# Kernel optimization log

Measured on AMD Instinct MI355X. Metric: run time of the kernel, lower is better.

## Reference

```python
import jax, jax.numpy as jnp
import numpy as np

WS, SHIFT, NH = 7, 3, 12

def _rel_pos_index(ws):
    coords = np.stack(np.meshgrid(np.arange(ws), np.arange(ws), indexing='ij'))  # [2,ws,ws]
    coords = coords.reshape(2, -1)
    rel = (coords[:, :, None] - coords[:, None, :]).transpose(1, 2, 0)  # [N,N,2]
    rel[:, :, 0] += ws - 1
    rel[:, :, 1] += ws - 1
    rel[:, :, 0] *= 2 * ws - 1
    return rel.sum(-1)  # [N,N] ints in [0,(2ws-1)^2)

def _attn_mask(H, W, ws, shift):
    img = np.zeros((H, W))
    cnt = 0
    for h in (slice(0, -ws), slice(-ws, -shift), slice(-shift, None)):
        for w in (slice(0, -ws), slice(-ws, -shift), slice(-shift, None)):
            img[h, w] = cnt
            cnt += 1
    mw = img.reshape(H // ws, ws, W // ws, ws).transpose(0, 2, 1, 3).reshape(-1, ws * ws)
    diff = mw[:, None, :] - mw[:, :, None]  # unsqueeze(1)-unsqueeze(2)
    return np.where(diff != 0, -100.0, 0.0).astype(np.float32)  # [nW,N,N]

def setup_inputs() -> dict:
    key = jax.random.key(0)
    ks = jax.random.split(key, 16)
    B, C, H, W = 16, 384, 56, 56
    hid = 4 * C
    s = 0.02
    return {
        'x': jax.random.normal(ks[0], (B, C, H, W), jnp.float32),
        'qkv_w': jax.random.normal(ks[1], (3 * C, C), jnp.float32) * s,
        'qkv_b': jnp.zeros((3 * C,), jnp.float32),
        'proj_w': jax.random.normal(ks[2], (C, C), jnp.float32) * s,
        'proj_b': jnp.zeros((C,), jnp.float32),
        'rpb': jax.random.normal(ks[3], ((2 * WS - 1) ** 2, NH), jnp.float32) * s,
        'norm1_w': jnp.ones((C,), jnp.float32),
        'norm1_b': jnp.zeros((C,), jnp.float32),
        'norm2_w': jnp.ones((C,), jnp.float32),
        'norm2_b': jnp.zeros((C,), jnp.float32),
        'fc1_w': jax.random.normal(ks[4], (hid, C), jnp.float32) * s,
        'fc1_b': jnp.zeros((hid,), jnp.float32),
        'fc2_w': jax.random.normal(ks[5], (C, hid), jnp.float32) * s,
        'fc2_b': jnp.zeros((C,), jnp.float32),
    }

def _ln(v, w, b):
    m = v.mean(-1, keepdims=True)
    var = ((v - m) ** 2).mean(-1, keepdims=True)
    return (v - m) / jnp.sqrt(var + 1e-5) * w + b

def reference(x, qkv_w, qkv_b, proj_w, proj_b, rpb, norm1_w, norm1_b, norm2_w, norm2_b, fc1_w, fc1_b, fc2_w, fc2_b):
    B, C, H, W = x.shape
    ws, shift, nh = WS, SHIFT, NH
    hd = C // nh
    scale = hd ** -0.5
    N = ws * ws
    nwh, nww = H // ws, W // ws
    xt = x.reshape(B, C, H * W).transpose(0, 2, 1)  # [B,L,C]
    shortcut = xt
    xn = _ln(xt, norm1_w, norm1_b).reshape(B, H, W, C)
    xs = jnp.roll(xn, (-shift, -shift), axis=(1, 2))
    win = xs.reshape(B, nwh, ws, nww, ws, C).transpose(0, 1, 3, 2, 4, 5).reshape(-1, N, C)
    qkv = (win @ qkv_w.T + qkv_b).reshape(-1, N, 3, nh, hd).transpose(2, 0, 3, 1, 4)
    q, k, v = qkv[0] * scale, qkv[1], qkv[2]  # [nWtot,nh,N,hd]
    attn = jnp.einsum('whnd,whmd->whnm', q, k)
    rpi = jnp.asarray(_rel_pos_index(ws))
    bias = rpb[rpi.reshape(-1)].reshape(N, N, nh).transpose(2, 0, 1)
    attn = attn + bias[None]
    mask = jnp.asarray(_attn_mask(H, W, ws, shift))  # [nW,N,N]
    nW = mask.shape[0]
    attn = attn.reshape(B, nW, nh, N, N) + mask[None, :, None]
    attn = jax.nn.softmax(attn.reshape(-1, nh, N, N), axis=-1)
    out = jnp.einsum('whnm,whmd->whnd', attn, v).transpose(0, 2, 1, 3).reshape(-1, N, C)
    out = out @ proj_w.T + proj_b
    out = out.reshape(B, nwh, nww, ws, ws, C).transpose(0, 1, 3, 2, 4, 5).reshape(B, H, W, C)
    out = jnp.roll(out, (shift, shift), axis=(1, 2)).reshape(B, H * W, C)
    xres = shortcut + out
    h = _ln(xres, norm2_w, norm2_b)
    h = jax.nn.gelu(h @ fc1_w.T + fc1_b, approximate=False)
    h = h @ fc2_w.T + fc2_b
    xout = xres + h
    return xout.transpose(0, 2, 1).reshape(B, C, H, W)
```

## Files before the change

### kernel.cpp

```cpp
#include <hip/hip_runtime.h>


using US   = unsigned short;
using bf8  = __attribute__((ext_vector_type(8))) short;
using f4   = __attribute__((ext_vector_type(4))) float;
using u4   = __attribute__((ext_vector_type(4))) unsigned int;
using u2   = __attribute__((ext_vector_type(2))) unsigned int;

__device__ __forceinline__ float b2f(US h){
  union { unsigned u; float f; } v; v.u = ((unsigned)h) << 16; return v.f;
}
__device__ __forceinline__ US f2b(float f){
  union { float f; unsigned u; } v; v.f = f;
  unsigned r = (v.u + 0x7FFFu + ((v.u >> 16) & 1u)) >> 16;
  return (US)r;
}
__device__ __forceinline__ unsigned cvt_pk_bf16(float lo, float hi){
  unsigned r;
  asm("v_cvt_pk_bf16_f32 %0, %1, %2" : "=v"(r) : "v"(lo), "v"(hi));
  return r;
}
__device__ __forceinline__ float rcp_f(float x){
  float r; asm("v_rcp_f32 %0, %1" : "=v"(r) : "v"(x)); return r;
}
__device__ __forceinline__ float exp2_f(float x){
  float r; asm("v_exp_f32 %0, %1" : "=v"(r) : "v"(x)); return r;
}
__device__ __forceinline__ float gelu_f(float x){
  float t = x*x;
  float m = x * (-2.3022082f - 0.1029434f*t);
  float e = exp2_f(m);
  return x * rcp_f(1.f + e);
}
__device__ __forceinline__ int xcd_seq(int n, int nwg){
  int q = nwg >> 3, r = nwg & 7;
  int xcd = n & 7, idx = n >> 3;
  int base = (xcd < r) ? xcd*(q+1) : (r + xcd*q);
  return base + idx;
}

__global__ void k_detect(const unsigned* __restrict__ n1w, int* __restrict__ flag){
  *flag = (n1w[0] == 0x3F803F80u) ? 1 : 0;
}

struct Ptrs { const void* p[13]; };
__constant__ const int g_cnt[13] = {442368,1152,147456,384,2028,384,384,384,384,589824,1536,589824,384};
__constant__ const int g_off[13] = {0,442368,443520,590976,591360,593408,593792,594176,594560,
                                    594944,1184768,1186304,1776128};

__global__ __launch_bounds__(256) void k_convert_all(Ptrs ptrs, US* __restrict__ dst,
                                                     const int* __restrict__ flag, int totpair){
  const int f = *flag;
  int g = blockIdx.x*256 + threadIdx.x;
  const int stride = gridDim.x*256;
  for (; g < totpair; g += stride){
    int i = 0, base = 0, off = 0;
    #pragma unroll
    for (int t = 0; t < 13; t++){
      int np = g_cnt[t] >> 1;
      if (g >= base && g < base + np){ i = t; off = base; }
      base += np;
    }
    int li = g - off;
    unsigned* d = (unsigned*)dst + (g_off[i] >> 1);
    if (f){
      d[li] = ((const unsigned*)ptrs.p[i])[li];
    } else {
      const float* s = (const float*)ptrs.p[i];
      unsigned lo = f2b(s[2*li]), hi = f2b(s[2*li+1]);
      d[li] = lo | (hi << 16);
    }
  }
}

__global__ __launch_bounds__(256) void k_transpose(const void* __restrict__ x, size_t xoff,
                                                   US* __restrict__ xt, const int* __restrict__ flag){
  __shared__ float tile[32][33];
  const int f = *flag;
  const int b = blockIdx.z;
  const int l0 = blockIdx.x * 32, c0 = blockIdx.y * 32;
  const int tx = threadIdx.x, ty = threadIdx.y;
  #pragma unroll
  for (int i = 0; i < 4; i++){
    int c = c0 + ty + i*8;
    size_t idx = xoff + ((size_t)b*384 + c)*3136 + l0 + tx;
    tile[ty + i*8][tx] = f ? b2f(((const US*)x)[idx]) : ((const float*)x)[idx];
  }
  __syncthreads();
  #pragma unroll
  for (int i = 0; i < 4; i++){
    int l = l0 + ty + i*8;
    xt[((size_t)b*3136 + l)*384 + c0 + tx] = f2b(tile[tx][ty + i*8]);
  }
}

__device__ __forceinline__ int win_row(int row){
  int b = row / 3136, l = row - b*3136;
  int ho = l / 56, wo = l - ho*56;
  int hs = ho - 3; if (hs < 0) hs += 56;
  int wsc = wo - 3; if (wsc < 0) wsc += 56;
  return ((b*8 + hs/7)*8 + wsc/7)*49 + (hs%7)*7 + (wsc%7);
}

__global__ __launch_bounds__(256) void k_ln1(const US* __restrict__ xt, const US* __restrict__ g,
                                             const US* __restrict__ bb, US* __restrict__ Xw){
  const int wv = threadIdx.x >> 6, lane = threadIdx.x & 63;
  const int row = blockIdx.x*4 + wv;
  const unsigned* src = (const unsigned*)(xt + (size_t)row*384);
  float v[6]; float s1 = 0.f, s2 = 0.f;
  #pragma unroll
  for (int k = 0; k < 3; k++){
    unsigned u = src[lane + 64*k];
    float lo = b2f((US)(u & 0xffff)), hi = b2f((US)(u >> 16));
    v[2*k] = lo; v[2*k+1] = hi;
    s1 += lo + hi; s2 += lo*lo + hi*hi;
  }
  #pragma unroll
  for (int off = 1; off < 64; off <<= 1){ s1 += __shfl_xor(s1, off); s2 += __shfl_xor(s2, off); }
  float mean = s1 * (1.f/384.f);
  float var  = s2 * (1.f/384.f) - mean*mean;
  float rstd = rsqrtf(var + 1e-5f);
  int r = win_row(row);
  unsigned* dst = (unsigned*)(Xw + (size_t)r*384);
  const unsigned* gw = (const unsigned*)g;
  const unsigned* gb = (const unsigned*)bb;
  #pragma unroll
  for (int k = 0; k < 3; k++){
    unsigned wg = gw[lane + 64*k], wb = gb[lane + 64*k];
    float o0 = (v[2*k]   - mean)*rstd*b2f((US)(wg & 0xffff)) + b2f((US)(wb & 0xffff));
    float o1 = (v[2*k+1] - mean)*rstd*b2f((US)(wg >> 16))    + b2f((US)(wb >> 16));
    dst[lane + 64*k] = cvt_pk_bf16(o0, o1);
  }
}

template<int EPI, int KT, int LDA>
__global__ __launch_bounds__(256) void k_gemm(const US* __restrict__ A, const US* __restrict__ Bw,
                                              const US* __restrict__ bias, US* __restrict__ C,
                                              int N){
  __shared__ __align__(16) US sh[128*128];
  US* Asl = sh;
  US* Bsl = sh + 8192;
  const int tid = threadIdx.x, wv = tid >> 6, lane = tid & 63;
  const int l16 = lane & 15, lq = lane >> 4;
  const int GX = gridDim.x, GY = gridDim.y;
  const int s  = xcd_seq(blockIdx.x + GX*blockIdx.y, GX*GY);
  const int bx = s / GY, by = s - bx*GY;
  const int row0 = bx * 128, col0 = by * 128;
  const int wr = (wv >> 1) * 64, wc = (wv & 1) * 64;
  f4 acc[4][4] = {};
  const int r8 = lane >> 3;
  const int c8 = lane & 7;
  const int csrc = c8 ^ r8;
  const US* ga = A  + (size_t)(row0 + wv*32 + r8)*LDA + csrc*8;
  const US* gb = Bw + (size_t)(col0 + wv*32 + r8)*KT  + csrc*8;
  US* lA = Asl + wv*2048;
  US* lB = Bsl + wv*2048;
  const int x7   = l16 & 7;
  #pragma unroll
  for (int k0 = 0; k0 < KT; k0 += 64){
    #pragma unroll
    for (int i = 0; i < 4; i++){
      __builtin_amdgcn_global_load_lds((__attribute__((address_space(1))) void*)(ga + k0 + (size_t)i*8*LDA),
                                       (__attribute__((address_space(3))) void*)(lA + i*512), 16, 0, 0);
      __builtin_amdgcn_global_load_lds((__attribute__((address_space(1))) void*)(gb + k0 + (size_t)i*8*KT),
                                       (__attribute__((address_space(3))) void*)(lB + i*512), 16, 0, 0);
    }
    __syncthreads();
    #pragma unroll
    for (int kk = 0; kk < 2; kk++){
      const int coff = (((kk << 2) | lq) ^ x7) * 8;
      bf8 af[4], bfr[4];
      #pragma unroll
      for (int m = 0; m < 4; m++) af[m]  = *(const bf8*)(Asl + (wr + m*16 + l16)*64 + coff);
      #pragma unroll
      for (int n = 0; n < 4; n++) bfr[n] = *(const bf8*)(Bsl + (wc + n*16 + l16)*64 + coff);
      #pragma unroll
      for (int n = 0; n < 4; n++)
        #pragma unroll
        for (int m = 0; m < 4; m++)
          acc[n][m] = __builtin_amdgcn_mfma_f32_16x16x32_bf16(bfr[n], af[m], acc[n][m], 0, 0, 0);
    }
    __syncthreads();
  }
  #pragma unroll
  for (int n = 0; n < 4; n++){
    const int colt = wc + n*16 + lq*4;
    const int colb = col0 + colt;
    u2 bw = *(const u2*)(bias + colb);
    float bv[4] = { b2f((US)(bw[0] & 0xffff)), b2f((US)(bw[0] >> 16)),
                    b2f((US)(bw[1] & 0xffff)), b2f((US)(bw[1] >> 16)) };
    #pragma unroll
    for (int m = 0; m < 4; m++){
      const int rowt = wr + m*16 + l16;
      float v[4];
      #pragma unroll
      for (int j = 0; j < 4; j++){
        float val = acc[n][m][j] + bv[j];
        if (EPI == 1){ if (colb < 384) val *= 0.17677669529663687f; }
        if (EPI == 2){ val = gelu_f(val); }
        v[j] = val;
      }
      u2 w;
      w[0] = cvt_pk_bf16(v[0], v[1]);
      w[1] = cvt_pk_bf16(v[2], v[3]);
      *(u2*)(sh + rowt*128 + (((colt >> 3) ^ (rowt & 15)) << 3) + (colt & 7)) = w;
    }
  }
  __syncthreads();
  const int cr = tid & 15, rb = tid >> 4;
  #pragma unroll
  for (int it = 0; it < 8; it++){
    const int r = rb + it*16;
    u4 v = *(const u4*)(sh + r*128 + ((cr ^ (r & 15)) << 3));
    *(u4*)(C + (size_t)(row0 + r)*N + col0 + cr*8) = v;
  }
}

__global__ __launch_bounds__(64) void k_attn(US* QKV, const US* __restrict__ rpb){
  const int s = xcd_seq(blockIdx.x + 12*blockIdx.y, 12*gridDim.y);
  const int win = s / 12, head = s - win*12;
  const int lane = threadIdx.x;
  const int l16 = lane & 15, lq = lane >> 4;
  __shared__ __align__(16) US ps[64*72];
  __shared__ float biasl[169];

  for (int i = lane; i < 169; i += 64) biasl[i] = b2f(rpb[i*12 + head]);
  __syncthreads();

  const size_t rowbase = (size_t)win * 49;
  const US* Qb = QKV + rowbase*1152 + head*32;

  bf8 qf[4], kf[4];
  #pragma unroll
  for (int m = 0; m < 4; m++){
    int row = m*16 + l16; if (row > 48) row = 48;
    const US* p = Qb + (size_t)row*1152 + lq*8;
    qf[m] = *(const bf8*)p;
    kf[m] = *(const bf8*)(p + 384);
  }

  const f4 zacc = {0.f, 0.f, 0.f, 0.f};
  f4 s4[4][4];
  #pragma unroll
  for (int m = 0; m < 4; m++)
    #pragma unroll
    for (int n = 0; n < 4; n++)
      s4[m][n] = __builtin_amdgcn_mfma_f32_16x16x32_bf16(qf[m], kf[n], zacc, 0, 0, 0);

  bf8 vf[2][2];
  #pragma unroll
  for (int kk = 0; kk < 2; kk++)
    #pragma unroll
    for (int i = 0; i < 8; i++){
      int key = kk*32 + lq*8 + i; if (key > 48) key = 48;
      const US* vp = Qb + (size_t)key*1152 + 768;
      vf[0][kk][i] = (short)vp[l16];
      vf[1][kk][i] = (short)vp[16 + l16];
    }

  const int wh = (win >> 3) & 7, ww = win & 7;
  int i2a[4], j2a[4], lblm[4]; bool vm[4];
  #pragma unroll
  for (int n = 0; n < 4; n++){
    int mk = n*16 + l16;
    vm[n] = (mk < 49);
    int mkc = vm[n] ? mk : 48;
    int i2 = mkc / 7, j2 = mkc - 7*i2;
    i2a[n] = i2; j2a[n] = j2;
    lblm[n] = ((wh == 7) ? (i2 < 4 ? 3 : 6) : 0) + ((ww == 7) ? (j2 < 4 ? 1 : 2) : 0);
  }

  float rinv[4][4];
  #pragma unroll
  for (int m = 0; m < 4; m++){
    #pragma unroll
    for (int j = 0; j < 4; j++){
      int nq = m*16 + lq*4 + j;
      int nqc = nq < 49 ? nq : 48;
      int i1 = nqc / 7, j1 = nqc - 7*i1;
      int lblq = ((wh == 7) ? (i1 < 4 ? 3 : 6) : 0) + ((ww == 7) ? (j1 < 4 ? 1 : 2) : 0);
      float vals[4];
      #pragma unroll
      for (int n = 0; n < 4; n++){
        int relidx = (i1 - i2a[n] + 6)*13 + (j1 - j2a[n] + 6);
        float t = s4[m][n][j] + biasl[relidx];
        if (lblq != lblm[n]) t -= 100.f;
        if (!vm[n]) t = -1e30f;
        vals[n] = t;
      }
      float mv = fmaxf(fmaxf(vals[0], vals[1]), fmaxf(vals[2], vals[3]));
      #pragma unroll
      for (int off = 1; off < 16; off <<= 1) mv = fmaxf(mv, __shfl_xor(mv, off));
      float sum = 0.f;
      #pragma unroll
      for (int n = 0; n < 4; n++){
        float p = vm[n] ? __expf(vals[n] - mv) : 0.f;
        sum += p;
        ps[(size_t)(m*16 + lq*4 + j)*72 + n*16 + l16] = f2b(p);
      }
      #pragma unroll
      for (int off = 1; off < 16; off <<= 1) sum += __shfl_xor(sum, off);
      rinv[m][j] = rcp_f(sum);
    }
  }
  __syncthreads();

  f4 o[4][2] = {};
  #pragma unroll
  for (int m = 0; m < 4; m++){
    #pragma unroll
    for (int kk = 0; kk < 2; kk++){
      bf8 pf = *(const bf8*)(ps + (size_t)(m*16 + l16)*72 + kk*32 + lq*8);
      #pragma unroll
      for (int nb = 0; nb < 2; nb++)
        o[m][nb] = __builtin_amdgcn_mfma_f32_16x16x32_bf16(pf, vf[nb][kk], o[m][nb], 0, 0, 0);
    }
  }
  #pragma unroll
  for (int m = 0; m < 4; m++)
    #pragma unroll
    for (int nb = 0; nb < 2; nb++)
      #pragma unroll
      for (int j = 0; j < 4; j++){
        int nq = m*16 + lq*4 + j;
        if (nq < 49){
          int d = nb*16 + l16;
          QKV[(rowbase + nq)*1152 + head*32 + d] = f2b(o[m][nb][j] * rinv[m][j]);
        }
      }
}

__global__ __launch_bounds__(256) void k_res_ln2(US* xt, const US* __restrict__ Y,
                                                 const US* __restrict__ g, const US* __restrict__ bb,
                                                 US* __restrict__ Xm){
  const int wv = threadIdx.x >> 6, lane = threadIdx.x & 63;
  const int row = blockIdx.x*4 + wv;
  int r = win_row(row);
  unsigned* sa = (unsigned*)(xt + (size_t)row*384);
  const unsigned* sy = (const unsigned*)(Y  + (size_t)r*384);
  unsigned* dm = (unsigned*)(Xm   + (size_t)row*384);
  float v[6]; float s1 = 0.f, s2 = 0.f;
  #pragma unroll
  for (int k = 0; k < 3; k++){
    unsigned ua = sa[lane + 64*k], uy = sy[lane + 64*k];
    float lo = b2f((US)(ua & 0xffff)) + b2f((US)(uy & 0xffff));
    float hi = b2f((US)(ua >> 16))    + b2f((US)(uy >> 16));
    v[2*k] = lo; v[2*k+1] = hi;
    s1 += lo + hi; s2 += lo*lo + hi*hi;
    sa[lane + 64*k] = cvt_pk_bf16(lo, hi);
  }
  #pragma unroll
  for (int off = 1; off < 64; off <<= 1){ s1 += __shfl_xor(s1, off); s2 += __shfl_xor(s2, off); }
  float mean = s1 * (1.f/384.f);
  float var  = s2 * (1.f/384.f) - mean*mean;
  float rstd = rsqrtf(var + 1e-5f);
  const unsigned* gw = (const unsigned*)g;
  const unsigned* gb = (const unsigned*)bb;
  #pragma unroll
  for (int k = 0; k < 3; k++){
    unsigned wg = gw[lane + 64*k], wb = gb[lane + 64*k];
    float o0 = (v[2*k]   - mean)*rstd*b2f((US)(wg & 0xffff)) + b2f((US)(wb & 0xffff));
    float o1 = (v[2*k+1] - mean)*rstd*b2f((US)(wg >> 16))    + b2f((US)(wb >> 16));
    dm[lane + 64*k] = cvt_pk_bf16(o0, o1);
  }
}

__global__ __launch_bounds__(256) void k_final(const US* __restrict__ xres, const US* __restrict__ Z,
                                               void* __restrict__ out, size_t ooff,
                                               const int* __restrict__ flag){
  __shared__ float tile[32][33];
  const int f = *flag;
  const int b = blockIdx.z;
  const int l0 = blockIdx.x * 32, c0 = blockIdx.y * 32;
  const int tx = threadIdx.x, ty = threadIdx.y;
  #pragma unroll
  for (int i = 0; i < 4; i++){
    int l = l0 + ty + i*8;
    size_t idx = ((size_t)b*3136 + l)*384 + c0 + tx;
    tile[ty + i*8][tx] = b2f(xres[idx]) + b2f(Z[idx]);
  }
  __syncthreads();
  #pragma unroll
  for (int i = 0; i < 4; i++){
    int c = c0 + ty + i*8;
    size_t idx = ooff + ((size_t)b*384 + c)*3136 + l0 + tx;
    float v = tile[tx][ty + i*8];
    if (f) ((US*)out)[idx] = f2b(v);
    else   ((float*)out)[idx] = v;
  }
}

extern "C" void kernel_launch(void* const* d_in, const int* in_sizes, int n_in,
                              void* d_out, int out_size, void* d_ws, size_t ws_size,
                              hipStream_t stream){
  char* w = (char*)d_ws;
  int* flag = (int*)w;
  US*  Wb   = (US*)(w + 256);

  const size_t O_QKVW=0, O_QKVB=442368, O_PROJW=443520, O_PROJB=590976, O_RPB=591360,
               O_N1W=593408, O_N1B=593792, O_N2W=594176, O_N2B=594560,
               O_FC1W=594944, O_FC1B=1184768, O_FC2W=1186304, O_FC2B=1776128;

  k_detect<<<1, 1, 0, stream>>>((const unsigned*)d_in[6], flag);
  {
    Ptrs ptrs;
    for (int i = 0; i < 13; i++) ptrs.p[i] = d_in[i+1];
    int totpair = (442368+1152+147456+384+2028+384*4+589824+1536+589824+384)/2;
    int grid = (totpair + 255)/256;
    k_convert_all<<<grid, 256, 0, stream>>>(ptrs, Wb, flag, totpair);
  }

  const size_t WOFF = 4ull<<20;
  const size_t U1 = 2408448ull;
  int NBC = 16;
  while (NBC > 4 && WOFF + 6ull*U1*(size_t)NBC > ws_size) NBC >>= 1;
  const size_t U  = U1 * (size_t)NBC;
  const int rows  = NBC * 3136;
  const int nchunks = 16 / NBC;

  char* cw = w + WOFF;
  US* xt  = (US*)(cw);
  US* Xw  = (US*)(cw + U);
  US* Xm  = Xw;
  US* QKV = (US*)(cw + 2*U);
  US* Hb  = (US*)(cw + 2*U);
  US* Zc  = (US*)(cw + 4*U);
  US* Y   = (US*)(cw + 5*U);

  dim3 bt(32, 8);
  for (int ch = 0; ch < nchunks; ch++){
    size_t eoff = (size_t)ch * NBC * 384 * 3136;
    k_transpose<<<dim3(98, 12, NBC), bt, 0, stream>>>(d_in[0], eoff, xt, flag);
    k_ln1<<<rows/4, 256, 0, stream>>>(xt, Wb+O_N1W, Wb+O_N1B, Xw);
    k_gemm<1,384,384><<<dim3(rows/128, 9), 256, 0, stream>>>(Xw, Wb+O_QKVW, Wb+O_QKVB, QKV, 1152);
    k_attn<<<dim3(12, NBC*64), 64, 0, stream>>>(QKV, Wb+O_RPB);
    k_gemm<0,384,1152><<<dim3(rows/128, 3), 256, 0, stream>>>(QKV, Wb+O_PROJW, Wb+O_PROJB, Y, 384);
    k_res_ln2<<<rows/4, 256, 0, stream>>>(xt, Y, Wb+O_N2W, Wb+O_N2B, Xm);
    const int Mh = rows / 2;
    for (int h = 0; h < 2; h++){
      k_gemm<2,384,384><<<dim3(Mh/128, 12), 256, 0, stream>>>(Xm + (size_t)h*Mh*384, Wb+O_FC1W, Wb+O_FC1B, Hb, 1536);
      k_gemm<0,1536,1536><<<dim3(Mh/128, 3), 256, 0, stream>>>(Hb, Wb+O_FC2W, Wb+O_FC2B, Zc + (size_t)h*Mh*384, 384);
    }
    k_final<<<dim3(98, 12, NBC), bt, 0, stream>>>(xt, Zc, d_out, eoff, flag);
  }
}
```

Measured before the change: 416.6 us.

## Fuse transpose with LN1, fold residual into proj epilogue, prescale Q weights

```diff
diff --git a/kernel.cpp b/kernel.cpp
--- a/kernel.cpp
+++ b/kernel.cpp
@@ -62,80 +62,83 @@
       base += np;
     }
     int li = g - off;
+    const bool qs = (i == 0 && li < 73728) || (i == 1 && li < 192);
+    const float sc = qs ? 0.17677669529663687f : 1.0f;
     unsigned* d = (unsigned*)dst + (g_off[i] >> 1);
     if (f){
-      d[li] = ((const unsigned*)ptrs.p[i])[li];
+      unsigned u = ((const unsigned*)ptrs.p[i])[li];
+      if (qs){
+        float lo = b2f((US)(u & 0xffff)) * sc, hi = b2f((US)(u >> 16)) * sc;
+        u = (unsigned)f2b(lo) | ((unsigned)f2b(hi) << 16);
+      }
+      d[li] = u;
     } else {
       const float* s = (const float*)ptrs.p[i];
-      unsigned lo = f2b(s[2*li]), hi = f2b(s[2*li+1]);
+      unsigned lo = f2b(s[2*li] * sc), hi = f2b(s[2*li+1] * sc);
       d[li] = lo | (hi << 16);
     }
   }
 }
 
-__global__ __launch_bounds__(256) void k_transpose(const void* __restrict__ x, size_t xoff,
-                                                   US* __restrict__ xt, const int* __restrict__ flag){
-  __shared__ float tile[32][33];
+__global__ __launch_bounds__(256) void k_pre(const void* __restrict__ x, size_t xoff,
+                                             US* __restrict__ xt, US* __restrict__ Xw,
+                                             const US* __restrict__ g, const US* __restrict__ bb,
+                                             const int* __restrict__ flag){
+  __shared__ float T[32][385];
   const int f = *flag;
-  const int b = blockIdx.z;
-  const int l0 = blockIdx.x * 32, c0 = blockIdx.y * 32;
+  const int b = blockIdx.y;
+  const int l0 = blockIdx.x * 32;
   const int tx = threadIdx.x, ty = threadIdx.y;
   #pragma unroll
-  for (int i = 0; i < 4; i++){
-    int c = c0 + ty + i*8;
-    size_t idx = xoff + ((size_t)b*384 + c)*3136 + l0 + tx;
-    tile[ty + i*8][tx] = f ? b2f(((const US*)x)[idx]) : ((const float*)x)[idx];
+  for (int cy = 0; cy < 12; cy++){
+    #pragma unroll
+    for (int i = 0; i < 4; i++){
+      int c = cy*32 + ty + i*8;
+      size_t idx = xoff + ((size_t)b*384 + c)*3136 + l0 + tx;
+      T[tx][c] = f ? b2f(((const US*)x)[idx]) : ((const float*)x)[idx];
+    }
   }
   __syncthreads();
-  #pragma unroll
-  for (int i = 0; i < 4; i++){
-    int l = l0 + ty + i*8;
-    xt[((size_t)b*3136 + l)*384 + c0 + tx] = f2b(tile[tx][ty + i*8]);
-  }
-}
-
-__device__ __forceinline__ int win_row(int row){
-  int b = row / 3136, l = row - b*3136;
-  int ho = l / 56, wo = l - ho*56;
-  int hs = ho - 3; if (hs < 0) hs += 56;
-  int wsc = wo - 3; if (wsc < 0) wsc += 56;
-  return ((b*8 + hs/7)*8 + wsc/7)*49 + (hs%7)*7 + (wsc%7);
-}
-
-__global__ __launch_bounds__(256) void k_ln1(const US* __restrict__ xt, const US* __restrict__ g,
-                                             const US* __restrict__ bb, US* __restrict__ Xw){
-  const int wv = threadIdx.x >> 6, lane = threadIdx.x & 63;
-  const int row = blockIdx.x*4 + wv;
-  const unsigned* src = (const unsigned*)(xt + (size_t)row*384);
-  float v[6]; float s1 = 0.f, s2 = 0.f;
-  #pragma unroll
-  for (int k = 0; k < 3; k++){
-    unsigned u = src[lane + 64*k];
-    float lo = b2f((US)(u & 0xffff)), hi = b2f((US)(u >> 16));
-    v[2*k] = lo; v[2*k+1] = hi;
-    s1 += lo + hi; s2 += lo*lo + hi*hi;
-  }
-  #pragma unroll
-  for (int off = 1; off < 64; off <<= 1){ s1 += __shfl_xor(s1, off); s2 += __shfl_xor(s2, off); }
-  float mean = s1 * (1.f/384.f);
-  float var  = s2 * (1.f/384.f) - mean*mean;
-  float rstd = rsqrtf(var + 1e-5f);
-  int r = win_row(row);
-  unsigned* dst = (unsigned*)(Xw + (size_t)r*384);
+  const int tid = ty*32 + tx;
+  const int wv = tid >> 6, lane = tid & 63;
   const unsigned* gw = (const unsigned*)g;
   const unsigned* gb = (const unsigned*)bb;
-  #pragma unroll
-  for (int k = 0; k < 3; k++){
-    unsigned wg = gw[lane + 64*k], wb = gb[lane + 64*k];
-    float o0 = (v[2*k]   - mean)*rstd*b2f((US)(wg & 0xffff)) + b2f((US)(wb & 0xffff));
-    float o1 = (v[2*k+1] - mean)*rstd*b2f((US)(wg >> 16))    + b2f((US)(wb >> 16));
-    dst[lane + 64*k] = cvt_pk_bf16(o0, o1);
+  for (int rr = 0; rr < 8; rr++){
+    const int row = wv*8 + rr;
+    const int l = l0 + row;
+    float v[6]; float s1 = 0.f, s2 = 0.f;
+    #pragma unroll
+    for (int k = 0; k < 3; k++){
+      float lo = T[row][2*(lane + 64*k)];
+      float hi = T[row][2*(lane + 64*k) + 1];
+      v[2*k] = lo; v[2*k+1] = hi;
+      s1 += lo + hi; s2 += lo*lo + hi*hi;
+    }
+    #pragma unroll
+    for (int off = 1; off < 64; off <<= 1){ s1 += __shfl_xor(s1, off); s2 += __shfl_xor(s2, off); }
+    float mean = s1 * (1.f/384.f);
+    float var  = s2 * (1.f/384.f) - mean*mean;
+    float rstd = rsqrtf(var + 1e-5f);
+    int ho = l / 56, wo = l - ho*56;
+    int hs = ho - 3; if (hs < 0) hs += 56;
+    int ws2 = wo - 3; if (ws2 < 0) ws2 += 56;
+    int r = ((b*8 + hs/7)*8 + ws2/7)*49 + (hs%7)*7 + (ws2%7);
+    unsigned* dx = (unsigned*)(xt + ((size_t)b*3136 + l)*384);
+    unsigned* dw = (unsigned*)(Xw + (size_t)r*384);
+    #pragma unroll
+    for (int k = 0; k < 3; k++){
+      unsigned wg = gw[lane + 64*k], wb = gb[lane + 64*k];
+      float o0 = (v[2*k]   - mean)*rstd*b2f((US)(wg & 0xffff)) + b2f((US)(wb & 0xffff));
+      float o1 = (v[2*k+1] - mean)*rstd*b2f((US)(wg >> 16))    + b2f((US)(wb >> 16));
+      dx[lane + 64*k] = cvt_pk_bf16(v[2*k], v[2*k+1]);
+      dw[lane + 64*k] = cvt_pk_bf16(o0, o1);
+    }
   }
 }
 
 template<int EPI, int KT, int LDA>
 __global__ __launch_bounds__(256) void k_gemm(const US* __restrict__ A, const US* __restrict__ Bw,
-                                              const US* __restrict__ bias, US* __restrict__ C,
+                                              const US* __restrict__ bias, US* C,
                                               int N){
   __shared__ __align__(16) US sh[128*128];
   US* Asl = sh;
@@ -155,7 +158,7 @@
   const US* gb = Bw + (size_t)(col0 + wv*32 + r8)*KT  + csrc*8;
   US* lA = Asl + wv*2048;
   US* lB = Bsl + wv*2048;
-  const int x7   = l16 & 7;
+  const int x7 = l16 & 7;
   #pragma unroll
   for (int k0 = 0; k0 < KT; k0 += 64){
     #pragma unroll
@@ -196,7 +199,6 @@
       #pragma unroll
       for (int j = 0; j < 4; j++){
         float val = acc[n][m][j] + bv[j];
-        if (EPI == 1){ if (colb < 384) val *= 0.17677669529663687f; }
         if (EPI == 2){ val = gelu_f(val); }
         v[j] = val;
       }
@@ -211,8 +213,28 @@
   #pragma unroll
   for (int it = 0; it < 8; it++){
     const int r = rb + it*16;
-    u4 v = *(const u4*)(sh + r*128 + ((cr ^ (r & 15)) << 3));
-    *(u4*)(C + (size_t)(row0 + r)*N + col0 + cr*8) = v;
+    u4 hv = *(const u4*)(sh + r*128 + ((cr ^ (r & 15)) << 3));
+    if (EPI == 3){
+      const int grow = row0 + r;
+      int win = grow / 49, nn = grow - win*49;
+      int bb2 = win >> 6, wh = (win >> 3) & 7, wwi = win & 7;
+      int ii = nn / 7, jj = nn - ii*7;
+      int ho = wh*7 + ii + 3; if (ho >= 56) ho -= 56;
+      int wo = wwi*7 + jj + 3; if (wo >= 56) wo -= 56;
+      size_t ir = (size_t)bb2*3136 + ho*56 + wo;
+      unsigned* xp = (unsigned*)(C + ir*384 + col0 + cr*8);
+      u4 xv = *(const u4*)xp;
+      u4 ov;
+      #pragma unroll
+      for (int q2 = 0; q2 < 4; q2++){
+        float a0 = b2f((US)(hv[q2] & 0xffff)) + b2f((US)(xv[q2] & 0xffff));
+        float a1 = b2f((US)(hv[q2] >> 16))    + b2f((US)(xv[q2] >> 16));
+        ov[q2] = cvt_pk_bf16(a0, a1);
+      }
+      *(u4*)xp = ov;
+    } else {
+      *(u4*)(C + (size_t)(row0 + r)*N + col0 + cr*8) = hv;
+    }
   }
 }
 
@@ -330,24 +352,20 @@
       }
 }
 
-__global__ __launch_bounds__(256) void k_res_ln2(US* xt, const US* __restrict__ Y,
-                                                 const US* __restrict__ g, const US* __restrict__ bb,
-                                                 US* __restrict__ Xm){
+__global__ __launch_bounds__(256) void k_ln2(const US* __restrict__ xres,
+                                             const US* __restrict__ g, const US* __restrict__ bb,
+                                             US* __restrict__ Xm){
   const int wv = threadIdx.x >> 6, lane = threadIdx.x & 63;
   const int row = blockIdx.x*4 + wv;
-  int r = win_row(row);
-  unsigned* sa = (unsigned*)(xt + (size_t)row*384);
-  const unsigned* sy = (const unsigned*)(Y  + (size_t)r*384);
-  unsigned* dm = (unsigned*)(Xm   + (size_t)row*384);
+  const unsigned* src = (const unsigned*)(xres + (size_t)row*384);
+  unsigned* dm = (unsigned*)(Xm + (size_t)row*384);
   float v[6]; float s1 = 0.f, s2 = 0.f;
   #pragma unroll
   for (int k = 0; k < 3; k++){
-    unsigned ua = sa[lane + 64*k], uy = sy[lane + 64*k];
-    float lo = b2f((US)(ua & 0xffff)) + b2f((US)(uy & 0xffff));
-    float hi = b2f((US)(ua >> 16))    + b2f((US)(uy >> 16));
+    unsigned u = src[lane + 64*k];
+    float lo = b2f((US)(u & 0xffff)), hi = b2f((US)(u >> 16));
     v[2*k] = lo; v[2*k+1] = hi;
     s1 += lo + hi; s2 += lo*lo + hi*hi;
-    sa[lane + 64*k] = cvt_pk_bf16(lo, hi);
   }
   #pragma unroll
   for (int off = 1; off < 64; off <<= 1){ s1 += __shfl_xor(s1, off); s2 += __shfl_xor(s2, off); }
@@ -413,7 +431,7 @@
   const size_t WOFF = 4ull<<20;
   const size_t U1 = 2408448ull;
   int NBC = 16;
-  while (NBC > 4 && WOFF + 6ull*U1*(size_t)NBC > ws_size) NBC >>= 1;
+  while (NBC > 4 && WOFF + 5ull*U1*(size_t)NBC > ws_size) NBC >>= 1;
   const size_t U  = U1 * (size_t)NBC;
   const int rows  = NBC * 3136;
   const int nchunks = 16 / NBC;
@@ -425,17 +443,15 @@
   US* QKV = (US*)(cw + 2*U);
   US* Hb  = (US*)(cw + 2*U);
   US* Zc  = (US*)(cw + 4*U);
-  US* Y   = (US*)(cw + 5*U);
 
   dim3 bt(32, 8);
   for (int ch = 0; ch < nchunks; ch++){
     size_t eoff = (size_t)ch * NBC * 384 * 3136;
-    k_transpose<<<dim3(98, 12, NBC), bt, 0, stream>>>(d_in[0], eoff, xt, flag);
-    k_ln1<<<rows/4, 256, 0, stream>>>(xt, Wb+O_N1W, Wb+O_N1B, Xw);
-    k_gemm<1,384,384><<<dim3(rows/128, 9), 256, 0, stream>>>(Xw, Wb+O_QKVW, Wb+O_QKVB, QKV, 1152);
+    k_pre<<<dim3(98, NBC), bt, 0, stream>>>(d_in[0], eoff, xt, Xw, Wb+O_N1W, Wb+O_N1B, flag);
+    k_gemm<0,384,384><<<dim3(rows/128, 9), 256, 0, stream>>>(Xw, Wb+O_QKVW, Wb+O_QKVB, QKV, 1152);
     k_attn<<<dim3(12, NBC*64), 64, 0, stream>>>(QKV, Wb+O_RPB);
-    k_gemm<0,384,1152><<<dim3(rows/128, 3), 256, 0, stream>>>(QKV, Wb+O_PROJW, Wb+O_PROJB, Y, 384);
-    k_res_ln2<<<rows/4, 256, 0, stream>>>(xt, Y, Wb+O_N2W, Wb+O_N2B, Xm);
+    k_gemm<3,384,1152><<<dim3(rows/128, 3), 256, 0, stream>>>(QKV, Wb+O_PROJW, Wb+O_PROJB, xt, 384);
+    k_ln2<<<rows/4, 256, 0, stream>>>(xt, Wb+O_N2W, Wb+O_N2B, Xm);
     const int Mh = rows / 2;
     for (int h = 0; h < 2; h++){
       k_gemm<2,384,384><<<dim3(Mh/128, 12), 256, 0, stream>>>(Xm + (size_t)h*Mh*384, Wb+O_FC1W, Wb+O_FC1B, Hb, 1536);
```

New measurement: 453.4 us. +8.8%, slower.
